# Kernel tuning notes

Hardware: AMD Instinct MI355X
Metric: run time of the kernel (lower is better)

Reference implementation:

```python
import jax, jax.numpy as jnp
import numpy as np
import math

EMSIZE = 1024
B, S = 4, 1024
N = B * S

def setup_inputs() -> dict:
    key = jax.random.key(0)
    k1, k2, k3, k4, k5 = jax.random.split(key, 5)
    x = jax.random.normal(k1, (B, S, EMSIZE), dtype=jnp.float32)
    mask = jax.random.randint(k2, (N, N), 0, 2, dtype=jnp.int32)
    # nn.Linear default init scale ~ 1/sqrt(fan_in); use small normal weights
    sc = 1.0 / math.sqrt(EMSIZE)
    Wq = jax.random.normal(k3, (EMSIZE, EMSIZE), dtype=jnp.float32) * sc
    Wk = jax.random.normal(k4, (EMSIZE, EMSIZE), dtype=jnp.float32) * sc
    Wv = jax.random.normal(k5, (EMSIZE, EMSIZE), dtype=jnp.float32) * sc
    return {"x": x, "mask": mask, "Wq": Wq, "Wk": Wk, "Wv": Wv}

def reference(x, mask, Wq, Wk, Wv):
    b, s, e = x.shape
    xf = x.reshape(b * s, e)                       # [N, E]
    q = xf @ Wq.T                                  # nn.Linear: x @ W^T
    k = xf @ Wk.T
    v = xf @ Wv.T
    sim = q @ k.T                                  # [N, N] full cross-batch scores
    sim = jnp.where(mask == 0, jnp.float32(-1e20), sim)
    # NOTE: original scales AFTER masking, matching masked_fill then divide
    attn = jax.nn.softmax(sim / math.sqrt(e), axis=-1)
    out = attn @ v                                 # [N, E]
    return out.reshape(b, s, e)
```

## Files before the change

kernel.cpp:

```cpp
#include <hip/hip_runtime.h>
#include <hip/hip_bf16.h>
#include <math.h>


typedef __attribute__((ext_vector_type(8))) __bf16 bf16x8;
typedef __attribute__((ext_vector_type(4))) __bf16 bf16x4;
typedef __attribute__((ext_vector_type(4))) float f32x4;

__device__ __forceinline__ void gload_lds16(const void* g, void* l) {
  __builtin_amdgcn_global_load_lds(
      (__attribute__((address_space(1))) void*)(g),
      (__attribute__((address_space(3))) void*)(l), 16, 0, 0);
}

#define WAITB(N) asm volatile("s_waitcnt vmcnt(" #N ")\ns_barrier" ::: "memory")

#define LDS_FRAG(base, r) \
  *(const bf16x8*)((base) + (r) * 32 + (((hi) ^ (((r) >> 1) & 3)) * 8))

#define MM16(mq, AF)                                                        \
  __builtin_amdgcn_s_setprio(1);                                            \
  _Pragma("unroll") for (int m = 0; m < 4; ++m)                             \
    _Pragma("unroll") for (int n = 0; n < 4; ++n)                           \
      acc[(mq) * 4 + m][n] = __builtin_amdgcn_mfma_f32_16x16x32_bf16(       \
          AF[m], bfr[n], acc[(mq) * 4 + m][n], 0, 0, 0);                    \
  __builtin_amdgcn_s_setprio(0);

template <int NT>
__device__ __forceinline__ void g8_loop(const __bf16* __restrict__ A, long lda, long row0,
                                        const __bf16* __restrict__ B, long ldb, long col0,
                                        int kt0, __bf16* sA, __bf16* sB,
                                        f32x4 (&acc)[8][4], int tid) {
  const int lane = tid & 63;
  const int w = tid >> 6;
  const int wr = w >> 2, wc = w & 3;
  const int lo = lane & 15, hi = lane >> 4;

  auto stageA = [&](int buf, int kt) {
#pragma unroll
    for (int j = 0; j < 2; ++j) {
      int p = tid + j * 512;
      int row = p >> 2, cg = (p & 3) ^ ((row >> 1) & 3);
      gload_lds16(A + (row0 + row) * lda + kt * 32 + cg * 8,
                  sA + buf * 8192 + p * 8);
    }
  };
  auto stageB = [&](int buf, int kt) {
#pragma unroll
    for (int j = 0; j < 2; ++j) {
      int p = tid + j * 512;
      int row = p >> 2, cg = (p & 3) ^ ((row >> 1) & 3);
      gload_lds16(B + (col0 + row) * ldb + kt * 32 + cg * 8,
                  sB + buf * 8192 + p * 8);
    }
  };

#pragma unroll
  for (int t = 0; t < 3; ++t) { stageA(t, kt0 + t); stageB(t, kt0 + t); }
  WAITB(8);

  for (int t = 0; t < NT; ++t) {
    const int d = t & 3;
    const __bf16* sAc = sA + d * 8192;
    const __bf16* sBc = sB + d * 8192;
    const int s = (t + 3) & 3;
    bf16x8 af[4], bfr[4];
#pragma unroll
    for (int m = 0; m < 4; ++m) af[m] = LDS_FRAG(sAc, wr * 128 + m * 16 + lo);
#pragma unroll
    for (int n = 0; n < 4; ++n) bfr[n] = LDS_FRAG(sBc, wc * 64 + n * 16 + lo);
    if (t + 3 < NT) stageA(s, kt0 + t + 3);
    __builtin_amdgcn_s_barrier();
    MM16(0, af);
    __builtin_amdgcn_s_barrier();
    bf16x8 af2[4];
#pragma unroll
    for (int m = 0; m < 4; ++m) af2[m] = LDS_FRAG(sAc, wr * 128 + 64 + m * 16 + lo);
    if (t + 3 < NT) stageB(s, kt0 + t + 3);
    __builtin_amdgcn_s_barrier();
    MM16(1, af2);
    if (t + 3 < NT)      { WAITB(8); }
    else if (t + 2 < NT) { WAITB(4); }
    else                 { WAITB(0); }
  }
}


__global__ __launch_bounds__(512) void qkv8(const __bf16* __restrict__ xb,
                                            const __bf16* __restrict__ wq,
                                            const __bf16* __restrict__ wk,
                                            const __bf16* __restrict__ wv,
                                            __bf16* __restrict__ qb,
                                            __bf16* __restrict__ kb,
                                            __bf16* __restrict__ vtb) {
  __shared__ __bf16 sA[4 * 8192];
  __shared__ __bf16 sB[4 * 8192];
  const int raw = blockIdx.x;
  const int wid = (raw & 7) * 24 + (raw >> 3);
  const int z = wid >> 6;
  const int r2 = wid & 63;
  const int tid = threadIdx.x;
  const __bf16* A;
  const __bf16* B;
  long row0, col0;
  if (z == 2) {
    A = wv; B = xb;
    row0 = (long)(r2 >> 4) * 256;
    col0 = (long)(r2 & 15) * 256;
  } else {
    A = xb; B = (z == 0) ? wq : wk;
    row0 = (long)(r2 >> 2) * 256;
    col0 = (long)(r2 & 3) * 256;
  }
  f32x4 acc[8][4] = {};
  g8_loop<32>(A, 1024, row0, B, 1024, col0, 0, sA, sB, acc, tid);

  const int lane = tid & 63, w = tid >> 6;
  const int wr = w >> 2, wc = w & 3;
  const int lo = lane & 15, hi = lane >> 4;
#pragma unroll
  for (int m = 0; m < 8; ++m)
#pragma unroll
    for (int n = 0; n < 4; ++n)
#pragma unroll
      for (int i = 0; i < 4; ++i) {
        long r = row0 + wr * 128 + m * 16 + hi * 4 + i;
        long c = col0 + wc * 64 + n * 16 + lo;
        __bf16 v = (__bf16)acc[m][n][i];
        if (z == 0)      qb[r * 1024 + c] = v;
        else if (z == 1) kb[r * 1024 + c] = v;
        else             vtb[r * 4096 + c] = v;
      }
}

__global__ __launch_bounds__(512) void qk8(const __bf16* __restrict__ qb,
                                           const __bf16* __restrict__ kb,
                                           __bf16* __restrict__ sim) {
  __shared__ __bf16 sA[4 * 8192];
  __shared__ __bf16 sB[4 * 8192];
  const int raw = blockIdx.x;
  const int wid = (raw & 7) * 32 + (raw >> 3);
  const long row0 = (long)(wid >> 4) * 256;
  const long col0 = (long)(wid & 15) * 256;
  const int tid = threadIdx.x;
  f32x4 acc[8][4] = {};
  g8_loop<32>(qb, 1024, row0, kb, 1024, col0, 0, sA, sB, acc, tid);

  const int lane = tid & 63, w = tid >> 6;
  const int wr = w >> 2, wc = w & 3;
  const int lo = lane & 15, hi = lane >> 4;
#pragma unroll
  for (int m = 0; m < 8; ++m)
#pragma unroll
    for (int n = 0; n < 4; ++n)
#pragma unroll
      for (int i = 0; i < 4; ++i) {
        long r = row0 + wr * 128 + m * 16 + hi * 4 + i;
        long c = col0 + wc * 64 + n * 16 + lo;
        sim[r * 4096 + c] = (__bf16)acc[m][n][i];
      }
}

__global__ __launch_bounds__(256) void pv4(const __bf16* __restrict__ attn,
                                           const __bf16* __restrict__ vt,
                                           float* __restrict__ out,
                                           float* __restrict__ p1) {
  __shared__ __bf16 sA[4 * 4096];
  __shared__ __bf16 sB[4 * 4096];
  const int raw = blockIdx.x;
  const int wid = (raw & 7) * 64 + (raw >> 3);
  const int z = wid >> 8;
  const int r2 = wid & 255;
  const long row0 = (long)(r2 >> 3) * 128;
  const long col0 = (long)(r2 & 7) * 128;
  float* C = z ? p1 : out;
  const int kt0 = z * 64;
  const int tid = threadIdx.x;
  const int lane = tid & 63, w = tid >> 6;
  const int wr = w >> 1, wc = w & 1;
  const int lo = lane & 15, hi = lane >> 4;
  constexpr int NT = 64;

  auto stageA = [&](int buf, int kt) {
#pragma unroll
    for (int j = 0; j < 2; ++j) {
      int p = tid + j * 256;
      int row = p >> 2, cg = (p & 3) ^ ((row >> 1) & 3);
      gload_lds16(attn + (row0 + row) * 4096 + kt * 32 + cg * 8,
                  sA + buf * 4096 + p * 8);
    }
  };
  auto stageB = [&](int buf, int kt) {
#pragma unroll
    for (int j = 0; j < 2; ++j) {
      int p = tid + j * 256;
      int row = p >> 2, cg = (p & 3) ^ ((row >> 1) & 3);
      gload_lds16(vt + (col0 + row) * 4096 + kt * 32 + cg * 8,
                  sB + buf * 4096 + p * 8);
    }
  };

  f32x4 acc[4][4] = {};
#pragma unroll
  for (int t = 0; t < 3; ++t) { stageA(t, kt0 + t); stageB(t, kt0 + t); }
  WAITB(8);

  for (int t = 0; t < NT; ++t) {
    const int d = t & 3;
    const __bf16* sAc = sA + d * 4096;
    const __bf16* sBc = sB + d * 4096;
    const int s = (t + 3) & 3;
    bf16x8 af[4], bfr[4];
#pragma unroll
    for (int m = 0; m < 4; ++m) af[m] = LDS_FRAG(sAc, wr * 64 + m * 16 + lo);
#pragma unroll
    for (int n = 0; n < 4; ++n) bfr[n] = LDS_FRAG(sBc, wc * 64 + n * 16 + lo);
    if (t + 3 < NT) { stageA(s, kt0 + t + 3); stageB(s, kt0 + t + 3); }
    __builtin_amdgcn_s_barrier();
    __builtin_amdgcn_s_setprio(1);
#pragma unroll
    for (int m = 0; m < 4; ++m)
#pragma unroll
      for (int n = 0; n < 4; ++n)
        acc[m][n] = __builtin_amdgcn_mfma_f32_16x16x32_bf16(af[m], bfr[n], acc[m][n], 0, 0, 0);
    __builtin_amdgcn_s_setprio(0);
    if (t + 3 < NT)      { WAITB(8); }
    else if (t + 2 < NT) { WAITB(4); }
    else                 { WAITB(0); }
  }

#pragma unroll
  for (int m = 0; m < 4; ++m)
#pragma unroll
    for (int n = 0; n < 4; ++n)
#pragma unroll
      for (int i = 0; i < 4; ++i) {
        long r = row0 + wr * 64 + m * 16 + hi * 4 + i;
        long c = col0 + wc * 64 + n * 16 + lo;
        C[r * 1024 + c] = acc[m][n][i];
      }
}

__global__ __launch_bounds__(256) void reduce_add2(float* __restrict__ out,
                                                   const float* __restrict__ p1) {
  int i = blockIdx.x * 256 + threadIdx.x;
  float4 a = ((const float4*)out)[i];
  float4 b = ((const float4*)p1)[i];
  a.x += b.x; a.y += b.y; a.z += b.z; a.w += b.w;
  ((float4*)out)[i] = a;
}

__global__ __launch_bounds__(256) void softmax_rows(__bf16* __restrict__ sim,
                                                    const int* __restrict__ mask) {
  const int row = blockIdx.x;
  __bf16* rp = sim + (size_t)row * 4096;
  const int4* mrow = (const int4*)(mask + (size_t)row * 4096);
  const int tid = threadIdx.x;

  float vals[16];
  float lmax = -INFINITY;
#pragma unroll
  for (int j = 0; j < 2; ++j) {
    bf16x8 s = ((const bf16x8*)rp)[tid + 256 * j];
    int4 m0 = mrow[(tid + 256 * j) * 2];
    int4 m1 = mrow[(tid + 256 * j) * 2 + 1];
    float f[8];
#pragma unroll
    for (int e = 0; e < 8; ++e) f[e] = (float)s[e];
    f[0] = m0.x ? f[0] : -1e20f;  f[1] = m0.y ? f[1] : -1e20f;
    f[2] = m0.z ? f[2] : -1e20f;  f[3] = m0.w ? f[3] : -1e20f;
    f[4] = m1.x ? f[4] : -1e20f;  f[5] = m1.y ? f[5] : -1e20f;
    f[6] = m1.z ? f[6] : -1e20f;  f[7] = m1.w ? f[7] : -1e20f;
#pragma unroll
    for (int e = 0; e < 8; ++e) {
      vals[8 * j + e] = f[e];
      lmax = fmaxf(lmax, f[e]);
    }
  }
#pragma unroll
  for (int off = 32; off; off >>= 1) lmax = fmaxf(lmax, __shfl_xor(lmax, off));
  __shared__ float red[4];
  __shared__ float bro[2];
  if ((tid & 63) == 0) red[tid >> 6] = lmax;
  __syncthreads();
  if (tid == 0) bro[0] = fmaxf(fmaxf(red[0], red[1]), fmaxf(red[2], red[3]));
  __syncthreads();
  const float m = bro[0];

  float e[16];
  float lsum = 0.f;
#pragma unroll
  for (int j = 0; j < 16; ++j) {
    e[j] = __expf((vals[j] - m) * 0.03125f);
    lsum += e[j];
  }
#pragma unroll
  for (int off = 32; off; off >>= 1) lsum += __shfl_xor(lsum, off);
  if ((tid & 63) == 0) red[tid >> 6] = lsum;
  __syncthreads();
  if (tid == 0) bro[1] = red[0] + red[1] + red[2] + red[3];
  __syncthreads();
  const float inv = 1.0f / bro[1];

#pragma unroll
  for (int j = 0; j < 2; ++j) {
    bf16x8 o;
#pragma unroll
    for (int q = 0; q < 8; ++q) o[q] = (__bf16)(e[8 * j + q] * inv);
    ((bf16x8*)rp)[tid + 256 * j] = o;
  }
}

__global__ __launch_bounds__(256) void cvt_all(const float* __restrict__ x,
                                               const float* __restrict__ wq,
                                               const float* __restrict__ wk,
                                               const float* __restrict__ wv,
                                               __bf16* __restrict__ xb,
                                               __bf16* __restrict__ wqb,
                                               __bf16* __restrict__ wkb,
                                               __bf16* __restrict__ wvb) {
  int b = blockIdx.x;
  const float* in;
  __bf16* out;
  int base;
  if (b < 4096)      { in = x;  out = xb;  base = b; }
  else if (b < 5120) { in = wq; out = wqb; base = b - 4096; }
  else if (b < 6144) { in = wk; out = wkb; base = b - 5120; }
  else               { in = wv; out = wvb; base = b - 6144; }
  int i = base * 256 + threadIdx.x;
  float4 f = ((const float4*)in)[i];
  bf16x4 o;
  o[0] = (__bf16)f.x; o[1] = (__bf16)f.y; o[2] = (__bf16)f.z; o[3] = (__bf16)f.w;
  ((bf16x4*)out)[i] = o;
}

extern "C" void kernel_launch(void* const* d_in, const int* in_sizes, int n_in,
                              void* d_out, int out_size, void* d_ws, size_t ws_size,
                              hipStream_t stream) {
  const float* x = (const float*)d_in[0];
  const int* mask = (const int*)d_in[1];
  const float* Wq = (const float*)d_in[2];
  const float* Wk = (const float*)d_in[3];
  const float* Wv = (const float*)d_in[4];
  float* out = (float*)d_out;

  char* ws = (char*)d_ws;
  __bf16* vtb = (__bf16*)(ws);
  __bf16* xb  = (__bf16*)(ws + (8ull << 20));
  __bf16* wqb = (__bf16*)(ws + (16ull << 20));
  __bf16* wkb = (__bf16*)(ws + (18ull << 20));
  __bf16* wvb = (__bf16*)(ws + (20ull << 20));
  __bf16* qb  = (__bf16*)(ws + (22ull << 20));
  __bf16* kb  = (__bf16*)(ws + (30ull << 20));
  __bf16* sim = (__bf16*)(ws + (38ull << 20));
  float*  p1  = (float*)(ws + (8ull << 20));

  cvt_all<<<7168, 256, 0, stream>>>(x, Wq, Wk, Wv, xb, wqb, wkb, wvb);

  qkv8<<<192, 512, 0, stream>>>(xb, wqb, wkb, wvb, qb, kb, vtb);
  qk8<<<256, 512, 0, stream>>>(qb, kb, sim);
  softmax_rows<<<4096, 256, 0, stream>>>(sim, mask);
  pv4<<<512, 256, 0, stream>>>(sim, vtb, out, p1);
  reduce_add2<<<4096, 256, 0, stream>>>(out, p1);
}
```

Baseline: 154.4 us.

## Restructure 256x256 GEMM mainloop to BK=64 double-buffer with split staging

The shared GEMM loop used by the QKV projection and QK^T kernels moves from a four-stage ring of K=32 tiles to a two-stage double buffer of K=64 tiles, with an 8-way XOR swizzle on 64-wide rows. Each iteration now runs four MFMA quadrants, reusing A and B fragments across them, and interleaves half-tile global-to-LDS stages between barrier-separated compute phases. This halves the iteration count and barrier/wait overhead per unit of K and aims to overlap loads with MFMA more evenly. The cost is more barriers per iteration and a shallower prefetch distance, which could expose memory latency.

```diff
diff --git a/kernel.cpp b/kernel.cpp
--- a/kernel.cpp
+++ b/kernel.cpp
@@ -14,74 +14,122 @@
 }
 
 #define WAITB(N) asm volatile("s_waitcnt vmcnt(" #N ")\ns_barrier" ::: "memory")
-
-#define LDS_FRAG(base, r) \
-  *(const bf16x8*)((base) + (r) * 32 + (((hi) ^ (((r) >> 1) & 3)) * 8))
-
-#define MM16(mq, AF)                                                        \
-  __builtin_amdgcn_s_setprio(1);                                            \
-  _Pragma("unroll") for (int m = 0; m < 4; ++m)                             \
-    _Pragma("unroll") for (int n = 0; n < 4; ++n)                           \
-      acc[(mq) * 4 + m][n] = __builtin_amdgcn_mfma_f32_16x16x32_bf16(       \
-          AF[m], bfr[n], acc[(mq) * 4 + m][n], 0, 0, 0);                    \
-  __builtin_amdgcn_s_setprio(0);
+#define BAR()    asm volatile("s_barrier" ::: "memory")
+#define MFMA_(a, b, c) __builtin_amdgcn_mfma_f32_16x16x32_bf16(a, b, c, 0, 0, 0)
+
+#define FRAG64(base, r, kk) \
+  *(const bf16x8*)((base) + (r) * 64 + (((((kk) >> 3) + hi) ^ ((r) & 7)) * 8))
 
 template <int NT>
-__device__ __forceinline__ void g8_loop(const __bf16* __restrict__ A, long lda, long row0,
-                                        const __bf16* __restrict__ B, long ldb, long col0,
-                                        int kt0, __bf16* sA, __bf16* sB,
-                                        f32x4 (&acc)[8][4], int tid) {
-  const int lane = tid & 63;
-  const int w = tid >> 6;
+__device__ __forceinline__ void g8m(const __bf16* __restrict__ A, long lda, long row0,
+                                    const __bf16* __restrict__ B, long ldb, long col0,
+                                    __bf16* sA, __bf16* sB,
+                                    f32x4 (&acc)[8][4], int tid) {
+  const int lane = tid & 63, w = tid >> 6;
   const int wr = w >> 2, wc = w & 3;
   const int lo = lane & 15, hi = lane >> 4;
 
-  auto stageA = [&](int buf, int kt) {
+  auto stA = [&](int buf, int t, int h) {
 #pragma unroll
     for (int j = 0; j < 2; ++j) {
       int p = tid + j * 512;
-      int row = p >> 2, cg = (p & 3) ^ ((row >> 1) & 3);
-      gload_lds16(A + (row0 + row) * lda + kt * 32 + cg * 8,
-                  sA + buf * 8192 + p * 8);
+      int rp = p >> 3, c = p & 7;
+      int arow = rp + (j ? 64 : 0) + (h ? 64 : 0);
+      int cg = c ^ (arow & 7);
+      gload_lds16(A + (row0 + arow) * lda + t * 64 + cg * 8,
+                  sA + buf * 16384 + arow * 64 + c * 8);
     }
   };
-  auto stageB = [&](int buf, int kt) {
+  auto stB = [&](int buf, int t, int h) {
 #pragma unroll
     for (int j = 0; j < 2; ++j) {
       int p = tid + j * 512;
-      int row = p >> 2, cg = (p & 3) ^ ((row >> 1) & 3);
-      gload_lds16(B + (col0 + row) * ldb + kt * 32 + cg * 8,
-                  sB + buf * 8192 + p * 8);
+      int rp = p >> 3, c = p & 7;
+      int arow = ((rp >> 5) << 6) + (rp & 31) + (h ? 32 : 0);
+      int cg = c ^ (arow & 7);
+      gload_lds16(B + (col0 + arow) * ldb + t * 64 + cg * 8,
+                  sB + buf * 16384 + arow * 64 + c * 8);
     }
   };
 
-#pragma unroll
-  for (int t = 0; t < 3; ++t) { stageA(t, kt0 + t); stageB(t, kt0 + t); }
-  WAITB(8);
+  stA(0, 0, 0); stA(0, 0, 1); stB(0, 0, 0); stB(0, 0, 1);
+  stA(1, 1, 0); stB(1, 1, 0); stB(1, 1, 1);
+  WAITB(6);
 
   for (int t = 0; t < NT; ++t) {
-    const int d = t & 3;
-    const __bf16* sAc = sA + d * 8192;
-    const __bf16* sBc = sB + d * 8192;
-    const int s = (t + 3) & 3;
-    bf16x8 af[4], bfr[4];
-#pragma unroll
-    for (int m = 0; m < 4; ++m) af[m] = LDS_FRAG(sAc, wr * 128 + m * 16 + lo);
-#pragma unroll
-    for (int n = 0; n < 4; ++n) bfr[n] = LDS_FRAG(sBc, wc * 64 + n * 16 + lo);
-    if (t + 3 < NT) stageA(s, kt0 + t + 3);
-    __builtin_amdgcn_s_barrier();
-    MM16(0, af);
-    __builtin_amdgcn_s_barrier();
-    bf16x8 af2[4];
-#pragma unroll
-    for (int m = 0; m < 4; ++m) af2[m] = LDS_FRAG(sAc, wr * 128 + 64 + m * 16 + lo);
-    if (t + 3 < NT) stageB(s, kt0 + t + 3);
-    __builtin_amdgcn_s_barrier();
-    MM16(1, af2);
-    if (t + 3 < NT)      { WAITB(8); }
-    else if (t + 2 < NT) { WAITB(4); }
-    else                 { WAITB(0); }
+    const int bf = t & 1;
+    const __bf16* sAc = sA + bf * 16384;
+    const __bf16* sBc = sB + bf * 16384;
+    bf16x8 a4[8], b01[4], b23[4];
+#pragma unroll
+    for (int m = 0; m < 4; ++m) {
+      a4[m * 2]     = FRAG64(sAc, wr * 128 + m * 16 + lo, 0);
+      a4[m * 2 + 1] = FRAG64(sAc, wr * 128 + m * 16 + lo, 32);
+    }
+#pragma unroll
+    for (int n = 0; n < 2; ++n) {
+      b01[n * 2]     = FRAG64(sBc, wc * 64 + n * 16 + lo, 0);
+      b01[n * 2 + 1] = FRAG64(sBc, wc * 64 + n * 16 + lo, 32);
+    }
+    if (t + 1 < NT) stA(bf ^ 1, t + 1, 1);
+    BAR();
+    __builtin_amdgcn_s_setprio(1);
+#pragma unroll
+    for (int m = 0; m < 4; ++m)
+#pragma unroll
+      for (int n = 0; n < 2; ++n) {
+        acc[m][n] = MFMA_(a4[m * 2], b01[n * 2], acc[m][n]);
+        acc[m][n] = MFMA_(a4[m * 2 + 1], b01[n * 2 + 1], acc[m][n]);
+      }
+    __builtin_amdgcn_s_setprio(0);
+    BAR();
+#pragma unroll
+    for (int n = 0; n < 2; ++n) {
+      b23[n * 2]     = FRAG64(sBc, wc * 64 + (n + 2) * 16 + lo, 0);
+      b23[n * 2 + 1] = FRAG64(sBc, wc * 64 + (n + 2) * 16 + lo, 32);
+    }
+    if (t + 2 < NT) stA(bf, t + 2, 0);
+    BAR();
+    __builtin_amdgcn_s_setprio(1);
+#pragma unroll
+    for (int m = 0; m < 4; ++m)
+#pragma unroll
+      for (int n = 0; n < 2; ++n) {
+        acc[m][n + 2] = MFMA_(a4[m * 2], b23[n * 2], acc[m][n + 2]);
+        acc[m][n + 2] = MFMA_(a4[m * 2 + 1], b23[n * 2 + 1], acc[m][n + 2]);
+      }
+    __builtin_amdgcn_s_setprio(0);
+    BAR();
+#pragma unroll
+    for (int m = 0; m < 4; ++m) {
+      a4[m * 2]     = FRAG64(sAc, wr * 128 + 64 + m * 16 + lo, 0);
+      a4[m * 2 + 1] = FRAG64(sAc, wr * 128 + 64 + m * 16 + lo, 32);
+    }
+    if (t + 2 < NT) stB(bf, t + 2, 0);
+    BAR();
+    __builtin_amdgcn_s_setprio(1);
+#pragma unroll
+    for (int m = 0; m < 4; ++m)
+#pragma unroll
+      for (int n = 0; n < 2; ++n) {
+        acc[4 + m][n] = MFMA_(a4[m * 2], b01[n * 2], acc[4 + m][n]);
+        acc[4 + m][n] = MFMA_(a4[m * 2 + 1], b01[n * 2 + 1], acc[4 + m][n]);
+      }
+    __builtin_amdgcn_s_setprio(0);
+    BAR();
+    if (t + 2 < NT) stB(bf, t + 2, 1);
+    BAR();
+    __builtin_amdgcn_s_setprio(1);
+#pragma unroll
+    for (int m = 0; m < 4; ++m)
+#pragma unroll
+      for (int n = 0; n < 2; ++n) {
+        acc[4 + m][n + 2] = MFMA_(a4[m * 2], b23[n * 2], acc[4 + m][n + 2]);
+        acc[4 + m][n + 2] = MFMA_(a4[m * 2 + 1], b23[n * 2 + 1], acc[4 + m][n + 2]);
+      }
+    __builtin_amdgcn_s_setprio(0);
+    if (t + 2 < NT) { WAITB(6); }
+    else            { WAITB(0); }
   }
 }
 
@@ -93,8 +141,8 @@
                                             __bf16* __restrict__ qb,
                                             __bf16* __restrict__ kb,
                                             __bf16* __restrict__ vtb) {
-  __shared__ __bf16 sA[4 * 8192];
-  __shared__ __bf16 sB[4 * 8192];
+  __shared__ __bf16 sA[2 * 16384];
+  __shared__ __bf16 sB[2 * 16384];
   const int raw = blockIdx.x;
   const int wid = (raw & 7) * 24 + (raw >> 3);
   const int z = wid >> 6;
@@ -113,7 +161,7 @@
     col0 = (long)(r2 & 3) * 256;
   }
   f32x4 acc[8][4] = {};
-  g8_loop<32>(A, 1024, row0, B, 1024, col0, 0, sA, sB, acc, tid);
+  g8m<16>(A, 1024, row0, B, 1024, col0, sA, sB, acc, tid);
 
   const int lane = tid & 63, w = tid >> 6;
   const int wr = w >> 2, wc = w & 3;
@@ -136,15 +184,15 @@
 __global__ __launch_bounds__(512) void qk8(const __bf16* __restrict__ qb,
                                            const __bf16* __restrict__ kb,
                                            __bf16* __restrict__ sim) {
-  __shared__ __bf16 sA[4 * 8192];
-  __shared__ __bf16 sB[4 * 8192];
+  __shared__ __bf16 sA[2 * 16384];
+  __shared__ __bf16 sB[2 * 16384];
   const int raw = blockIdx.x;
   const int wid = (raw & 7) * 32 + (raw >> 3);
   const long row0 = (long)(wid >> 4) * 256;
   const long col0 = (long)(wid & 15) * 256;
   const int tid = threadIdx.x;
   f32x4 acc[8][4] = {};
-  g8_loop<32>(qb, 1024, row0, kb, 1024, col0, 0, sA, sB, acc, tid);
+  g8m<16>(qb, 1024, row0, kb, 1024, col0, sA, sB, acc, tid);
 
   const int lane = tid & 63, w = tid >> 6;
   const int wr = w >> 2, wc = w & 3;
@@ -160,6 +208,9 @@
         sim[r * 4096 + c] = (__bf16)acc[m][n][i];
       }
 }
+
+#define LDS_FRAG32(base, r) \
+  *(const bf16x8*)((base) + (r) * 32 + (((hi) ^ (((r) >> 1) & 3)) * 8))
 
 __global__ __launch_bounds__(256) void pv4(const __bf16* __restrict__ attn,
                                            const __bf16* __restrict__ vt,
@@ -212,9 +263,9 @@
     const int s = (t + 3) & 3;
     bf16x8 af[4], bfr[4];
 #pragma unroll
-    for (int m = 0; m < 4; ++m) af[m] = LDS_FRAG(sAc, wr * 64 + m * 16 + lo);
-#pragma unroll
-    for (int n = 0; n < 4; ++n) bfr[n] = LDS_FRAG(sBc, wc * 64 + n * 16 + lo);
+    for (int m = 0; m < 4; ++m) af[m] = LDS_FRAG32(sAc, wr * 64 + m * 16 + lo);
+#pragma unroll
+    for (int n = 0; n < 4; ++n) bfr[n] = LDS_FRAG32(sBc, wc * 64 + n * 16 + lo);
     if (t + 3 < NT) { stageA(s, kt0 + t + 3); stageB(s, kt0 + t + 3); }
     __builtin_amdgcn_s_barrier();
     __builtin_amdgcn_s_setprio(1);
@@ -222,7 +273,7 @@
     for (int m = 0; m < 4; ++m)
 #pragma unroll
       for (int n = 0; n < 4; ++n)
-        acc[m][n] = __builtin_amdgcn_mfma_f32_16x16x32_bf16(af[m], bfr[n], acc[m][n], 0, 0, 0);
+        acc[m][n] = MFMA_(af[m], bfr[n], acc[m][n]);
     __builtin_amdgcn_s_setprio(0);
     if (t + 3 < NT)      { WAITB(8); }
     else if (t + 2 < NT) { WAITB(4); }
```

New measurement: 154.6 us. About the same (+0.1%).
